# Kernel optimization log

Hardware: AMD Instinct MI355X
Metric: run time of the kernel (lower is better)

## Reference

```python
import jax, jax.numpy as jnp
import numpy as np

B, NC, RF, D, H, L = 32, 36, 16, 1024, 8, 2  # batch, compressed tokens, rf tokens, hidden, heads, layers
DFF = 4 * D
EPS = 1e-5


def _ln(x, s, b):
    m = jnp.mean(x, axis=-1, keepdims=True)
    v = jnp.mean((x - m) ** 2, axis=-1, keepdims=True)
    return (x - m) * jax.lax.rsqrt(v + EPS) * s + b


def setup_inputs() -> dict:
    key = jax.random.key(0)
    ks = jax.random.split(key, 8)
    s = 0.02
    return {
        "compressed_tokens": jax.random.normal(ks[0], (B, NC, D), dtype=jnp.float32),
        "rf_queries": jax.random.normal(ks[1], (RF, D), dtype=jnp.float32) * s,
        "ln1_s": jnp.ones((L, D), jnp.float32), "ln1_b": jnp.zeros((L, D), jnp.float32),
        "wq": jax.random.normal(ks[2], (L, D, D), dtype=jnp.float32) * s,
        "bq": jnp.zeros((L, D), jnp.float32),
        "wk": jax.random.normal(ks[3], (L, D, D), dtype=jnp.float32) * s,
        "bk": jnp.zeros((L, D), jnp.float32),
        "wv": jax.random.normal(ks[4], (L, D, D), dtype=jnp.float32) * s,
        "bv": jnp.zeros((L, D), jnp.float32),
        "wo": jax.random.normal(ks[5], (L, D, D), dtype=jnp.float32) * s,
        "bo": jnp.zeros((L, D), jnp.float32),
        "ln2_s": jnp.ones((L, D), jnp.float32), "ln2_b": jnp.zeros((L, D), jnp.float32),
        "w1": jax.random.normal(ks[6], (L, D, DFF), dtype=jnp.float32) * s,
        "b1": jnp.zeros((L, DFF), jnp.float32),
        "w2": jax.random.normal(ks[7], (L, DFF, D), dtype=jnp.float32) * s,
        "b2": jnp.zeros((L, D), jnp.float32),
        "lnf_s": jnp.ones((D,), jnp.float32), "lnf_b": jnp.zeros((D,), jnp.float32),
    }


def reference(compressed_tokens, rf_queries, ln1_s, ln1_b, wq, bq, wk, bk, wv, bv,
              wo, bo, ln2_s, ln2_b, w1, b1, w2, b2, lnf_s, lnf_b):
    Bv, NCv, Dv = compressed_tokens.shape
    N = Bv * NCv
    dh = Dv // H
    scale = 1.0 / float(np.sqrt(dh))
    x = jnp.broadcast_to(rf_queries[None], (N, RF, Dv))   # (N, 16, D)
    kv = compressed_tokens.reshape(N, 1, Dv)              # (N, 1, D)
    for i in range(L):
        # cross-attention (kv_len = 1)
        qn = _ln(x, ln1_s[i], ln1_b[i])
        q = (qn @ wq[i] + bq[i]).reshape(N, RF, H, dh)
        k = (kv @ wk[i] + bk[i]).reshape(N, 1, H, dh)
        v = (kv @ wv[i] + bv[i]).reshape(N, 1, H, dh)
        scores = jnp.einsum('nqhd,nkhd->nhqk', q, k) * scale
        attn = jax.nn.softmax(scores, axis=-1)            # trivially ones for kv_len=1
        ao = jnp.einsum('nhqk,nkhd->nqhd', attn, v).reshape(N, RF, Dv)
        x = x + ao @ wo[i] + bo[i]
        # MLP
        h = _ln(x, ln2_s[i], ln2_b[i])
        h = jax.nn.gelu(h @ w1[i] + b1[i], approximate=False)
        x = x + h @ w2[i] + b2[i]
    x = _ln(x, lnf_s, lnf_b)
    return x.reshape(Bv, NCv, RF, Dv)
```

## Files before the change

kernel.cpp:

```cpp
#include <hip/hip_runtime.h>
#include <hip/hip_bf16.h>
#include <math.h>

typedef float f4 __attribute__((ext_vector_type(4)));
typedef float f32x4 __attribute__((ext_vector_type(4)));
typedef _Float16 h4 __attribute__((ext_vector_type(4)));
typedef _Float16 h8 __attribute__((ext_vector_type(8)));

#define D_ 1024
#define DFF_ 4096
#define L_ 2
#define RF_ 16
#define NTOK_ 1152
#define M_ 18432
#define XROWS_ 1280

__device__ __forceinline__ void gload_lds16(const void* g, void* l) {
  __builtin_amdgcn_global_load_lds((const __attribute__((address_space(1))) void*)g,
                                   (__attribute__((address_space(3))) void*)l, 16, 0, 0);
}

__device__ __forceinline__ float gelu_f(float x) {
  float z = fabsf(x) * 0.70710678118654752f;
  float t = 1.0f / (1.0f + 0.3275911f * z);
  float poly = t * (0.254829592f + t * (-0.284496736f + t * (1.421413741f +
               t * (-1.453152027f + t * 1.061405429f))));
  float erfz = 1.0f - poly * __expf(-z * z);
  erfz = copysignf(erfz, x);
  return 0.5f * x * (1.0f + erfz);
}

__global__ __launch_bounds__(256) void k_init_x(float* __restrict__ x, const float* __restrict__ rfq) {
  int i = blockIdx.x * 256 + threadIdx.x;
  int c = i & 255;
  int m = i >> 8;
  ((f4*)x)[i] = ((const f4*)rfq)[((m & 15) << 8) | c];
}

__global__ __launch_bounds__(256) void k_cvt(const float* __restrict__ in, _Float16* __restrict__ out) {
  int i = blockIdx.x * 256 + threadIdx.x;
  f4 v = ((const f4*)in)[i];
  ((h4*)out)[i] = __builtin_convertvector(v, h4);
}

__global__ __launch_bounds__(256) void k_bcast_add(float* __restrict__ x, const float* __restrict__ att) {
  int i = blockIdx.x * 256 + threadIdx.x;
  int c = i & 255;
  int m = i >> 8;
  int n = m >> 4;
  f4 v = ((f4*)x)[i];
  f4 a = ((const f4*)att)[(n << 8) | c];
  ((f4*)x)[i] = v + a;
}

__global__ __launch_bounds__(256) void k_build_X(const float* __restrict__ att, const float* __restrict__ rfq,
                                                 const float* __restrict__ s, const float* __restrict__ b,
                                                 _Float16* __restrict__ X) {
  int i = blockIdx.x * 256 + threadIdx.x;
  int c = i & 255;
  int row = i >> 8;
  f4 sv = ((const f4*)s)[c];
  f4 v;
  if (row < 1152)      v = ((const f4*)att)[(row << 8) | c] * sv;
  else if (row < 1168) v = ((const f4*)rfq)[((row - 1152) << 8) | c] * sv;
  else if (row == 1168) v = sv;
  else if (row == 1169) v = ((const f4*)b)[c];
  else                 v = (f4){0.f, 0.f, 0.f, 0.f};
  ((h4*)X)[i] = __builtin_convertvector(v, h4);
}

__global__ __launch_bounds__(256) void k_transpose_cvt(const float* __restrict__ W, _Float16* __restrict__ WT,
                                                       int R, int C) {
  __shared__ float t[32][33];
  int c0 = blockIdx.x * 32, r0 = blockIdx.y * 32;
  int cc = threadIdx.x & 31, rr = threadIdx.x >> 5;
  #pragma unroll
  for (int p = 0; p < 32; p += 8)
    t[rr + p][cc] = W[(size_t)(r0 + rr + p) * C + (c0 + cc)];
  __syncthreads();
  #pragma unroll
  for (int p = 0; p < 32; p += 8)
    WT[(size_t)(c0 + rr + p) * R + (r0 + cc)] = (_Float16)t[cc][rr + p];
}

__device__ inline float block_sum256(float v) {
  __shared__ float red[4];
  #pragma unroll
  for (int o = 32; o > 0; o >>= 1) v += __shfl_down(v, o);
  int w = threadIdx.x >> 6;
  if ((threadIdx.x & 63) == 0) red[w] = v;
  __syncthreads();
  float r = red[0] + red[1] + red[2] + red[3];
  __syncthreads();
  return r;
}

__global__ __launch_bounds__(256) void k_scal_n(const float* __restrict__ att, const float* __restrict__ rfq,
                                                float* __restrict__ out) {
  int n = blockIdx.x;
  int t = threadIdx.x;
  f4 av = ((const f4*)(att + (size_t)n * D_))[t];
  float s1 = block_sum256(av.x + av.y + av.z + av.w);
  float s2 = block_sum256(av.x*av.x + av.y*av.y + av.z*av.z + av.w*av.w);
  if (t == 0) { out[n*24+0] = s1; out[n*24+1] = s2; }
  #pragma unroll
  for (int r = 0; r < RF_; ++r) {
    f4 qv = ((const f4*)(rfq + (size_t)r * D_))[t];
    float d = block_sum256(av.x*qv.x + av.y*qv.y + av.z*qv.z + av.w*qv.w);
    if (t == 0) out[n*24+2+r] = d;
  }
}

__global__ __launch_bounds__(256) void k_scal_q(const float* __restrict__ rfq, float* __restrict__ out) {
  int r = blockIdx.x;
  int t = threadIdx.x;
  f4 qv = ((const f4*)(rfq + (size_t)r * D_))[t];
  float s1 = block_sum256(qv.x + qv.y + qv.z + qv.w);
  float s2 = block_sum256(qv.x*qv.x + qv.y*qv.y + qv.z*qv.z + qv.w*qv.w);
  if (t == 0) { out[r*2+0] = s1; out[r*2+1] = s2; }
}

__global__ __launch_bounds__(256) void k_combine_gelu(const float* __restrict__ P,
                                                      const float* __restrict__ scn,
                                                      const float* __restrict__ scq,
                                                      const float* __restrict__ b1,
                                                      _Float16* __restrict__ H1, int m0) {
  int m = m0 + blockIdx.x;
  int n = m >> 4, r = m & 15;
  float Sa = scn[n*24+0], Saa = scn[n*24+1], dq = scn[n*24+2+r];
  float Sq = scq[r*2+0], Sqq = scq[r*2+1];
  float mu  = (Sa + Sq) * (1.0f / D_);
  float ex2 = (Saa + 2.0f*dq + Sqq) * (1.0f / D_);
  float rstd = rsqrtf(ex2 - mu*mu + 1e-5f);
  const f4* Pa = (const f4*)(P + (size_t)n * DFF_);
  const f4* Pq = (const f4*)(P + (size_t)(1152 + r) * DFF_);
  const f4* Ps = (const f4*)(P + (size_t)1168 * DFF_);
  const f4* Pb = (const f4*)(P + (size_t)1169 * DFF_);
  const f4* B1 = (const f4*)b1;
  h4* out = (h4*)(H1 + (size_t)blockIdx.x * DFF_);
  #pragma unroll
  for (int it = 0; it < 4; ++it) {
    int j = threadIdx.x + (it << 8);
    f4 hp = (Pa[j] + Pq[j] - mu * Ps[j]) * rstd + Pb[j] + B1[j];
    h4 o;
    o.x = (_Float16)gelu_f(hp.x); o.y = (_Float16)gelu_f(hp.y);
    o.z = (_Float16)gelu_f(hp.z); o.w = (_Float16)gelu_f(hp.w);
    out[j] = o;
  }
}

template<int F16OUT>
__global__ __launch_bounds__(256) void k_ln(const float* __restrict__ x, const float* __restrict__ s,
                                            const float* __restrict__ b, void* __restrict__ out) {
  size_t row = blockIdx.x;
  int t = threadIdx.x;
  f4 v = ((const f4*)(x + row * D_))[t];
  float mean = block_sum256(v.x + v.y + v.z + v.w) * (1.0f / D_);
  f4 d = v - mean;
  float var = block_sum256(d.x*d.x + d.y*d.y + d.z*d.z + d.w*d.w) * (1.0f / D_);
  float rstd = rsqrtf(var + 1e-5f);
  f4 sc = ((const f4*)s)[t];
  f4 bb = ((const f4*)b)[t];
  f4 r = d * rstd * sc + bb;
  if (F16OUT) ((h4*)out)[row * (D_/4) + t] = __builtin_convertvector(r, h4);
  else        ((f4*)out)[row * (D_/4) + t] = r;
}

template<int EPI, int K, int N>
__global__ __launch_bounds__(256) void k_gemm(const _Float16* __restrict__ A,
                                              const _Float16* __restrict__ Bt,
                                              const float* __restrict__ bias,
                                              void* __restrict__ out, int M) {
  __shared__ __align__(16) _Float16 As[128][64];
  __shared__ __align__(16) _Float16 Bs[128][64];
  const int tid = threadIdx.x;
  const int lane = tid & 63;
  const int w = tid >> 6;

  const unsigned gdx = gridDim.x;
  const unsigned nwg = gdx * gridDim.y;
  unsigned bid = blockIdx.y * gdx + blockIdx.x;
  if ((nwg & 7u) == 0u) bid = (bid & 7u) * (nwg >> 3) + (bid >> 3);
  const int bm = (int)(bid / gdx) << 7;
  const int bn = (int)(bid % gdx) << 7;

  const int wr = (w >> 1) << 6;
  const int wc = (w & 1) << 6;
  const int g = lane >> 4;
  const int lr = lane & 15;
  const int x7 = lr & 7;
  const int srow = lane >> 3;
  const int scl8 = (((lane & 7) ^ (srow & 7)) << 3);
  const int c8a = ((0 + g) ^ x7) << 3;
  const int c8b = ((4 + g) ^ x7) << 3;

  f32x4 acc[4][4];
  #pragma unroll
  for (int m = 0; m < 4; ++m)
    #pragma unroll
    for (int n = 0; n < 4; ++n)
      acc[m][n] = (f32x4){0.f, 0.f, 0.f, 0.f};

  const _Float16* gA = A + (size_t)(bm + (w << 5) + srow) * K + scl8;
  const _Float16* gB = Bt + (size_t)(bn + (w << 5) + srow) * K + scl8;

  for (int kt = 0; kt < K; kt += 64) {
    #pragma unroll
    for (int p = 0; p < 4; ++p) {
      const int r0 = (w << 5) + (p << 3);
      gload_lds16(gA + p * (K << 3), &As[r0][0]);
      gload_lds16(gB + p * (K << 3), &Bs[r0][0]);
    }
    gA += 64; gB += 64;
    __syncthreads();
    #pragma unroll
    for (int s2 = 0; s2 < 2; ++s2) {
      const int c8 = s2 ? c8b : c8a;
      h8 af[4], bf[4];
      #pragma unroll
      for (int m = 0; m < 4; ++m) af[m] = *(const h8*)(&As[wr + (m << 4) + lr][c8]);
      #pragma unroll
      for (int n = 0; n < 4; ++n) bf[n] = *(const h8*)(&Bs[wc + (n << 4) + lr][c8]);
      #pragma unroll
      for (int m = 0; m < 4; ++m)
        #pragma unroll
        for (int n = 0; n < 4; ++n)
          acc[m][n] = __builtin_amdgcn_mfma_f32_16x16x32_f16(af[m], bf[n], acc[m][n], 0, 0, 0);
    }
    __syncthreads();
  }

  #pragma unroll
  for (int n = 0; n < 4; ++n) {
    int col = bn + wc + (n << 4) + lr;
    float bval = (EPI == 4) ? 0.0f : bias[col];
    #pragma unroll
    for (int m = 0; m < 4; ++m) {
      #pragma unroll
      for (int j = 0; j < 4; ++j) {
        int row = bm + wr + (m << 4) + (g << 2) + j;
        float v = acc[m][n][j] + bval;
        size_t off = (size_t)row * N + col;
        if constexpr (EPI == 0)      ((_Float16*)out)[off] = (_Float16)v;
        else if constexpr (EPI == 1) ((float*)out)[off] = v;
        else if constexpr (EPI == 2) ((_Float16*)out)[off] = (_Float16)gelu_f(v);
        else if constexpr (EPI == 3) ((float*)out)[off] += v;
        else                         ((float*)out)[off] = v;
      }
    }
  }
}

template<int EPI, int K, int N>
__global__ __launch_bounds__(512, 2) void k_gemm256(const _Float16* __restrict__ A,
                                                    const _Float16* __restrict__ Bt,
                                                    const float* __restrict__ bias,
                                                    void* __restrict__ out) {
  __shared__ __align__(16) _Float16 sm[3][2][256][32];
  const int tid = threadIdx.x;
  const int lane = tid & 63;
  const int w = tid >> 6;
  const int wrow = w >> 2;
  const int wcol = w & 3;

  const unsigned gdx = gridDim.x;
  const unsigned nwg = gdx * gridDim.y;
  unsigned bid = blockIdx.y * gdx + blockIdx.x;
  if ((nwg & 7u) == 0u) bid = (bid & 7u) * (nwg >> 3) + (bid >> 3);
  const int bm = (int)(bid / gdx) << 8;
  const int bn = (int)(bid % gdx) << 8;

  const int g  = lane >> 4;
  const int lr = lane & 15;
  const int x3 = lr & 3;
  const int ps = (g ^ x3) << 3;
  const int srow = lane >> 2;
  const int scl4 = ((lane & 3) ^ (srow & 3)) << 3;

  f32x4 acc[8][4];
  #pragma unroll
  for (int i = 0; i < 8; ++i)
    #pragma unroll
    for (int j = 0; j < 4; ++j) acc[i][j] = (f32x4){0.f, 0.f, 0.f, 0.f};

  const _Float16* sA = A  + (size_t)(bm + (w << 5) + srow) * K + scl4;
  const _Float16* sB = Bt + (size_t)(bn + (w << 5) + srow) * K + scl4;
  const int NT = K >> 5;

  auto stageA = [&](int u) {
    _Float16* d = &sm[u % 3][0][w << 5][0];
    gload_lds16(sA + u * 32,          d);
    gload_lds16(sA + u * 32 + 16 * K, d + 16 * 32);
  };
  auto stageB = [&](int u) {
    _Float16* d = &sm[u % 3][1][w << 5][0];
    gload_lds16(sB + u * 32,          d);
    gload_lds16(sB + u * 32 + 16 * K, d + 16 * 32);
  };

  stageA(0); stageB(0); stageA(1); stageB(1);
  asm volatile("s_waitcnt vmcnt(4)" ::: "memory");
  __builtin_amdgcn_s_barrier();

  for (int t = 0; t < NT; ++t) {
    const int b = t % 3;
    h8 af[4], bfc[4];
    #pragma unroll
    for (int r = 0; r < 4; ++r) af[r]  = *(const h8*)(&sm[b][0][(wrow << 7) + (r << 4) + lr][ps]);
    #pragma unroll
    for (int c = 0; c < 4; ++c) bfc[c] = *(const h8*)(&sm[b][1][(wcol << 6) + (c << 4) + lr][ps]);
    if (t + 2 < NT) stageA(t + 2);
    __builtin_amdgcn_s_setprio(1);
    #pragma unroll
    for (int r = 0; r < 4; ++r)
      #pragma unroll
      for (int c = 0; c < 4; ++c)
        acc[r][c] = __builtin_amdgcn_mfma_f32_16x16x32_f16(af[r], bfc[c], acc[r][c], 0, 0, 0);
    __builtin_amdgcn_s_setprio(0);
    #pragma unroll
    for (int r = 0; r < 4; ++r) af[r] = *(const h8*)(&sm[b][0][(wrow << 7) + 64 + (r << 4) + lr][ps]);
    if (t + 2 < NT) stageB(t + 2);
    __builtin_amdgcn_s_setprio(1);
    #pragma unroll
    for (int r = 0; r < 4; ++r)
      #pragma unroll
      for (int c = 0; c < 4; ++c)
        acc[4 + r][c] = __builtin_amdgcn_mfma_f32_16x16x32_f16(af[r], bfc[c], acc[4 + r][c], 0, 0, 0);
    __builtin_amdgcn_s_setprio(0);
    asm volatile("s_waitcnt lgkmcnt(0)" ::: "memory");
    if (t + 2 < NT) { asm volatile("s_waitcnt vmcnt(4)" ::: "memory"); }
    else            { asm volatile("s_waitcnt vmcnt(0)" ::: "memory"); }
    __builtin_amdgcn_s_barrier();
  }

  #pragma unroll
  for (int c = 0; c < 4; ++c) {
    int col = bn + (wcol << 6) + (c << 4) + lr;
    float bval = bias[col];
    #pragma unroll
    for (int rf = 0; rf < 8; ++rf) {
      #pragma unroll
      for (int j = 0; j < 4; ++j) {
        int row = bm + (wrow << 7) + (rf << 4) + (g << 2) + j;
        float v = acc[rf][c][j] + bval;
        size_t off = (size_t)row * N + col;
        if constexpr (EPI == 2) ((_Float16*)out)[off] = (_Float16)gelu_f(v);
        else                    ((float*)out)[off] += v;
      }
    }
  }
}

extern "C" void kernel_launch(void* const* d_in, const int* in_sizes, int n_in,
                              void* d_out, int out_size, void* d_ws, size_t ws_size,
                              hipStream_t stream) {
  const float* ct   = (const float*)d_in[0];
  const float* rfq  = (const float*)d_in[1];
  const float* wv   = (const float*)d_in[8];
  const float* bv   = (const float*)d_in[9];
  const float* wo   = (const float*)d_in[10];
  const float* bo   = (const float*)d_in[11];
  const float* ln2s = (const float*)d_in[12];
  const float* ln2b = (const float*)d_in[13];
  const float* w1   = (const float*)d_in[14];
  const float* b1   = (const float*)d_in[15];
  const float* w2   = (const float*)d_in[16];
  const float* b2   = (const float*)d_in[17];
  const float* lnfs = (const float*)d_in[18];
  const float* lnfb = (const float*)d_in[19];

  float* x = (float*)d_out;

  char* p = (char*)d_ws;
  auto alloc = [&](size_t bytes) { char* r = p; p += (bytes + 255) & ~(size_t)255; return r; };
  _Float16* kvh = (_Float16*)alloc((size_t)NTOK_ * D_ * 2);
  _Float16* Vh  = (_Float16*)alloc((size_t)NTOK_ * D_ * 2);
  float*    att = (float*)   alloc((size_t)NTOK_ * D_ * 4);
  _Float16* wvt = (_Float16*)alloc((size_t)D_ * D_ * 2);
  _Float16* wot = (_Float16*)alloc((size_t)D_ * D_ * 2);
  _Float16* w1t = (_Float16*)alloc((size_t)D_ * DFF_ * 2);
  _Float16* w2t = (_Float16*)alloc((size_t)DFF_ * D_ * 2);
  _Float16* Xh  = (_Float16*)alloc((size_t)XROWS_ * D_ * 2);
  float*    P   = (float*)   alloc((size_t)XROWS_ * DFF_ * 4);
  float*    scn = (float*)   alloc((size_t)NTOK_ * 24 * 4);
  float*    scq = (float*)   alloc((size_t)RF_ * 2 * 4);
  size_t persist = (size_t)(p - (char*)d_ws);

  int MC = 1152;
  const int cand[4] = {9216, 4608, 2304, 1152};
  for (int i = 0; i < 4; ++i) {
    size_t need = persist + ((size_t)cand[i] * D_ * 2 + 256) + ((size_t)cand[i] * DFF_ * 2 + 256) + 1024;
    if (need <= ws_size) { MC = cand[i]; break; }
  }
  _Float16* hh  = (_Float16*)alloc((size_t)MC * D_ * 2);
  _Float16* H1h = (_Float16*)alloc((size_t)MC * DFF_ * 2);
  const bool use256 = (MC % 256 == 0);

  k_init_x<<<M_ * D_ / 4 / 256, 256, 0, stream>>>(x, rfq);
  k_cvt<<<NTOK_ * D_ / 4 / 256, 256, 0, stream>>>(ct, kvh);

  for (int l = 0; l < L_; ++l) {
    k_transpose_cvt<<<dim3(D_/32, D_/32), 256, 0, stream>>>(wv + (size_t)l*D_*D_,   wvt, D_, D_);
    k_transpose_cvt<<<dim3(D_/32, D_/32), 256, 0, stream>>>(wo + (size_t)l*D_*D_,   wot, D_, D_);
    k_transpose_cvt<<<dim3(DFF_/32, D_/32), 256, 0, stream>>>(w1 + (size_t)l*D_*DFF_, w1t, D_, DFF_);
    k_transpose_cvt<<<dim3(D_/32, DFF_/32), 256, 0, stream>>>(w2 + (size_t)l*DFF_*D_, w2t, DFF_, D_);

    k_gemm<0,1024,1024><<<dim3(D_/128, NTOK_/128), 256, 0, stream>>>(kvh, wvt, bv + l*D_, Vh, NTOK_);
    k_gemm<1,1024,1024><<<dim3(D_/128, NTOK_/128), 256, 0, stream>>>(Vh,  wot, bo + l*D_, att, NTOK_);
    k_bcast_add<<<M_ * D_ / 4 / 256, 256, 0, stream>>>(x, att);

    if (l == 0) {
      k_build_X<<<XROWS_ * D_ / 4 / 256, 256, 0, stream>>>(att, rfq, ln2s, ln2b, Xh);
      k_scal_n<<<NTOK_, 256, 0, stream>>>(att, rfq, scn);
      k_scal_q<<<RF_, 256, 0, stream>>>(rfq, scq);
      k_gemm<4,1024,4096><<<dim3(DFF_/128, XROWS_/128), 256, 0, stream>>>(Xh, w1t, nullptr, P, XROWS_);
      for (int m0 = 0; m0 < M_; m0 += MC) {
        k_combine_gelu<<<MC, 256, 0, stream>>>(P, scn, scq, b1, H1h, m0);
        if (use256)
          k_gemm256<3,4096,1024><<<dim3(D_/256, MC/256), 512, 0, stream>>>(H1h, w2t, b2, x + (size_t)m0 * D_);
        else
          k_gemm<3,4096,1024><<<dim3(D_/128, MC/128), 256, 0, stream>>>(H1h, w2t, b2, x + (size_t)m0 * D_, MC);
      }
    } else {
      for (int m0 = 0; m0 < M_; m0 += MC) {
        k_ln<1><<<MC, 256, 0, stream>>>(x + (size_t)m0 * D_, ln2s + l*D_, ln2b + l*D_, hh);
        if (use256) {
          k_gemm256<2,1024,4096><<<dim3(DFF_/256, MC/256), 512, 0, stream>>>(hh,  w1t, b1 + l*DFF_, H1h);
          k_gemm256<3,4096,1024><<<dim3(D_/256, MC/256), 512, 0, stream>>>(H1h, w2t, b2 + l*D_, x + (size_t)m0 * D_);
        } else {
          k_gemm<2,1024,4096><<<dim3(DFF_/128, MC/128), 256, 0, stream>>>(hh,  w1t, b1 + l*DFF_, H1h, MC);
          k_gemm<3,4096,1024><<<dim3(D_/128, MC/128), 256, 0, stream>>>(H1h, w2t, b2 + l*D_, x + (size_t)m0 * D_, MC);
        }
      }
    }
  }
  k_ln<0><<<M_, 256, 0, stream>>>(x, lnfs, lnfb, d_out);
}
```

Before: 1.011 ms.

## Restructure 256-row GEMM with K=64 double buffering and selectable N tile

The 256x256 MFMA GEMM is reworked to use 64-wide K tiles with double-buffered LDS and an 8-way XOR swizzle. It adds a templated N tile width (BN), and the down-projection GEMM (N=1024) now uses 256x128 tiles to launch twice as many workgroups. Each K step is split into four MFMA phases separated by barriers, with the A and B global-to-LDS loads staggered across them. The extra barriers and the shallower two-stage pipeline could cost more in synchronisation than the larger K tile saves.

```diff
diff --git a/kernel.cpp b/kernel.cpp
--- a/kernel.cpp
+++ b/kernel.cpp
@@ -251,97 +251,135 @@
   }
 }
 
-template<int EPI, int K, int N>
+template<int EPI, int K, int N, int BN>
 __global__ __launch_bounds__(512, 2) void k_gemm256(const _Float16* __restrict__ A,
                                                     const _Float16* __restrict__ Bt,
                                                     const float* __restrict__ bias,
                                                     void* __restrict__ out) {
-  __shared__ __align__(16) _Float16 sm[3][2][256][32];
+  constexpr int WN = BN / 64;
+  constexpr int WM = 8 / WN;
+  constexpr int WR = 256 / WM;
+  constexpr int RFN = WR / 16;
+  constexpr int HF = RFN / 2;
+  constexpr int nB = BN / 64;
+  __shared__ __align__(16) _Float16 As[2][256][64];
+  __shared__ __align__(16) _Float16 Bs[2][BN][64];
+
   const int tid = threadIdx.x;
   const int lane = tid & 63;
   const int w = tid >> 6;
-  const int wrow = w >> 2;
-  const int wcol = w & 3;
+  const int wm = w / WN, wn = w % WN;
 
   const unsigned gdx = gridDim.x;
   const unsigned nwg = gdx * gridDim.y;
   unsigned bid = blockIdx.y * gdx + blockIdx.x;
   if ((nwg & 7u) == 0u) bid = (bid & 7u) * (nwg >> 3) + (bid >> 3);
   const int bm = (int)(bid / gdx) << 8;
-  const int bn = (int)(bid % gdx) << 8;
+  const int bn = (int)(bid % gdx) * BN;
 
   const int g  = lane >> 4;
   const int lr = lane & 15;
-  const int x3 = lr & 3;
-  const int ps = (g ^ x3) << 3;
-  const int srow = lane >> 2;
-  const int scl4 = ((lane & 3) ^ (srow & 3)) << 3;
-
-  f32x4 acc[8][4];
-  #pragma unroll
-  for (int i = 0; i < 8; ++i)
+  const int x7 = lr & 7;
+  const int ps0 = (g ^ x7) << 3;
+  const int ps1 = ((4 | g) ^ x7) << 3;
+  const int srow = lane >> 3;
+  const int scl8 = ((lane & 7) ^ srow) << 3;
+
+  f32x4 acc[RFN][4];
+  #pragma unroll
+  for (int i = 0; i < RFN; ++i)
     #pragma unroll
     for (int j = 0; j < 4; ++j) acc[i][j] = (f32x4){0.f, 0.f, 0.f, 0.f};
 
-  const _Float16* sA = A  + (size_t)(bm + (w << 5) + srow) * K + scl4;
-  const _Float16* sB = Bt + (size_t)(bn + (w << 5) + srow) * K + scl4;
-  const int NT = K >> 5;
-
-  auto stageA = [&](int u) {
-    _Float16* d = &sm[u % 3][0][w << 5][0];
-    gload_lds16(sA + u * 32,          d);
-    gload_lds16(sA + u * 32 + 16 * K, d + 16 * 32);
+  const _Float16* srcA = A  + (size_t)(bm + (w << 5) + srow) * K + scl8;
+  const _Float16* srcB = Bt + (size_t)(bn + w * (BN >> 3) + srow) * K + scl8;
+
+  auto stageA = [&](int buf, int kt) {
+    #pragma unroll
+    for (int p = 0; p < 4; ++p)
+      gload_lds16(srcA + (size_t)(p << 3) * K + kt, &As[buf][(w << 5) + (p << 3)][0]);
   };
-  auto stageB = [&](int u) {
-    _Float16* d = &sm[u % 3][1][w << 5][0];
-    gload_lds16(sB + u * 32,          d);
-    gload_lds16(sB + u * 32 + 16 * K, d + 16 * 32);
+  auto stageB = [&](int buf, int kt) {
+    #pragma unroll
+    for (int p = 0; p < nB; ++p)
+      gload_lds16(srcB + (size_t)(p << 3) * K + kt, &Bs[buf][w * (BN >> 3) + (p << 3)][0]);
   };
-
-  stageA(0); stageB(0); stageA(1); stageB(1);
-  asm volatile("s_waitcnt vmcnt(4)" ::: "memory");
+  auto vwait = [&](bool deep) {
+    if (deep) { if constexpr (nB == 4) asm volatile("s_waitcnt vmcnt(4)" ::: "memory");
+                else                   asm volatile("s_waitcnt vmcnt(2)" ::: "memory"); }
+    else      asm volatile("s_waitcnt vmcnt(0)" ::: "memory");
+  };
+
+  const int NT = K >> 6;
+  stageA(0, 0); stageB(0, 0); stageB(1, 64);
+  vwait(true);
   __builtin_amdgcn_s_barrier();
 
+  h8 af[HF], bfc[4];
   for (int t = 0; t < NT; ++t) {
-    const int b = t % 3;
-    h8 af[4], bfc[4];
-    #pragma unroll
-    for (int r = 0; r < 4; ++r) af[r]  = *(const h8*)(&sm[b][0][(wrow << 7) + (r << 4) + lr][ps]);
-    #pragma unroll
-    for (int c = 0; c < 4; ++c) bfc[c] = *(const h8*)(&sm[b][1][(wcol << 6) + (c << 4) + lr][ps]);
-    if (t + 2 < NT) stageA(t + 2);
+    const int buf = t & 1;
+    #pragma unroll
+    for (int r = 0; r < HF; ++r) af[r] = *(const h8*)(&As[buf][wm * WR + (r << 4) + lr][ps0]);
+    #pragma unroll
+    for (int c = 0; c < 4; ++c) bfc[c] = *(const h8*)(&Bs[buf][wn * 64 + (c << 4) + lr][ps0]);
+    if (t + 1 < NT) stageA(buf ^ 1, (t + 1) << 6);
+    __builtin_amdgcn_s_barrier();
     __builtin_amdgcn_s_setprio(1);
     #pragma unroll
-    for (int r = 0; r < 4; ++r)
+    for (int r = 0; r < HF; ++r)
       #pragma unroll
       for (int c = 0; c < 4; ++c)
         acc[r][c] = __builtin_amdgcn_mfma_f32_16x16x32_f16(af[r], bfc[c], acc[r][c], 0, 0, 0);
     __builtin_amdgcn_s_setprio(0);
-    #pragma unroll
-    for (int r = 0; r < 4; ++r) af[r] = *(const h8*)(&sm[b][0][(wrow << 7) + 64 + (r << 4) + lr][ps]);
-    if (t + 2 < NT) stageB(t + 2);
+    __builtin_amdgcn_s_barrier();
+    #pragma unroll
+    for (int r = 0; r < HF; ++r) af[r] = *(const h8*)(&As[buf][wm * WR + ((HF + r) << 4) + lr][ps0]);
+    __builtin_amdgcn_s_barrier();
     __builtin_amdgcn_s_setprio(1);
     #pragma unroll
-    for (int r = 0; r < 4; ++r)
+    for (int r = 0; r < HF; ++r)
       #pragma unroll
       for (int c = 0; c < 4; ++c)
-        acc[4 + r][c] = __builtin_amdgcn_mfma_f32_16x16x32_f16(af[r], bfc[c], acc[4 + r][c], 0, 0, 0);
+        acc[HF + r][c] = __builtin_amdgcn_mfma_f32_16x16x32_f16(af[r], bfc[c], acc[HF + r][c], 0, 0, 0);
     __builtin_amdgcn_s_setprio(0);
-    asm volatile("s_waitcnt lgkmcnt(0)" ::: "memory");
-    if (t + 2 < NT) { asm volatile("s_waitcnt vmcnt(4)" ::: "memory"); }
-    else            { asm volatile("s_waitcnt vmcnt(0)" ::: "memory"); }
+    __builtin_amdgcn_s_barrier();
+    #pragma unroll
+    for (int r = 0; r < HF; ++r) af[r] = *(const h8*)(&As[buf][wm * WR + (r << 4) + lr][ps1]);
+    #pragma unroll
+    for (int c = 0; c < 4; ++c) bfc[c] = *(const h8*)(&Bs[buf][wn * 64 + (c << 4) + lr][ps1]);
+    __builtin_amdgcn_s_barrier();
+    __builtin_amdgcn_s_setprio(1);
+    #pragma unroll
+    for (int r = 0; r < HF; ++r)
+      #pragma unroll
+      for (int c = 0; c < 4; ++c)
+        acc[r][c] = __builtin_amdgcn_mfma_f32_16x16x32_f16(af[r], bfc[c], acc[r][c], 0, 0, 0);
+    __builtin_amdgcn_s_setprio(0);
+    __builtin_amdgcn_s_barrier();
+    #pragma unroll
+    for (int r = 0; r < HF; ++r) af[r] = *(const h8*)(&As[buf][wm * WR + ((HF + r) << 4) + lr][ps1]);
+    if (t + 2 < NT) stageB(buf, (t + 2) << 6);
+    __builtin_amdgcn_s_barrier();
+    __builtin_amdgcn_s_setprio(1);
+    #pragma unroll
+    for (int r = 0; r < HF; ++r)
+      #pragma unroll
+      for (int c = 0; c < 4; ++c)
+        acc[HF + r][c] = __builtin_amdgcn_mfma_f32_16x16x32_f16(af[r], bfc[c], acc[HF + r][c], 0, 0, 0);
+    __builtin_amdgcn_s_setprio(0);
+    vwait(t + 2 < NT);
     __builtin_amdgcn_s_barrier();
   }
 
   #pragma unroll
   for (int c = 0; c < 4; ++c) {
-    int col = bn + (wcol << 6) + (c << 4) + lr;
+    int col = bn + wn * 64 + (c << 4) + lr;
     float bval = bias[col];
     #pragma unroll
-    for (int rf = 0; rf < 8; ++rf) {
+    for (int rf = 0; rf < RFN; ++rf) {
       #pragma unroll
       for (int j = 0; j < 4; ++j) {
-        int row = bm + (wrow << 7) + (rf << 4) + (g << 2) + j;
+        int row = bm + wm * WR + (rf << 4) + (g << 2) + j;
         float v = acc[rf][c][j] + bval;
         size_t off = (size_t)row * N + col;
         if constexpr (EPI == 2) ((_Float16*)out)[off] = (_Float16)gelu_f(v);
@@ -417,7 +455,7 @@
       for (int m0 = 0; m0 < M_; m0 += MC) {
         k_combine_gelu<<<MC, 256, 0, stream>>>(P, scn, scq, b1, H1h, m0);
         if (use256)
-          k_gemm256<3,4096,1024><<<dim3(D_/256, MC/256), 512, 0, stream>>>(H1h, w2t, b2, x + (size_t)m0 * D_);
+          k_gemm256<3,4096,1024,128><<<dim3(D_/128, MC/256), 512, 0, stream>>>(H1h, w2t, b2, x + (size_t)m0 * D_);
         else
           k_gemm<3,4096,1024><<<dim3(D_/128, MC/128), 256, 0, stream>>>(H1h, w2t, b2, x + (size_t)m0 * D_, MC);
       }
@@ -425,8 +463,8 @@
       for (int m0 = 0; m0 < M_; m0 += MC) {
         k_ln<1><<<MC, 256, 0, stream>>>(x + (size_t)m0 * D_, ln2s + l*D_, ln2b + l*D_, hh);
         if (use256) {
-          k_gemm256<2,1024,4096><<<dim3(DFF_/256, MC/256), 512, 0, stream>>>(hh,  w1t, b1 + l*DFF_, H1h);
-          k_gemm256<3,4096,1024><<<dim3(D_/256, MC/256), 512, 0, stream>>>(H1h, w2t, b2 + l*D_, x + (size_t)m0 * D_);
+          k_gemm256<2,1024,4096,256><<<dim3(DFF_/256, MC/256), 512, 0, stream>>>(hh,  w1t, b1 + l*DFF_, H1h);
+          k_gemm256<3,4096,1024,128><<<dim3(D_/128, MC/256), 512, 0, stream>>>(H1h, w2t, b2 + l*D_, x + (size_t)m0 * D_);
         } else {
           k_gemm<2,1024,4096><<<dim3(DFF_/128, MC/128), 256, 0, stream>>>(hh,  w1t, b1 + l*DFF_, H1h, MC);
           k_gemm<3,4096,1024><<<dim3(D_/128, MC/128), 256, 0, stream>>>(H1h, w2t, b2 + l*D_, x + (size_t)m0 * D_, MC);
```

Measured after the change: 1.306 ms. 29.2% more time.
